# Kernel tuning notes

Hardware: AMD Instinct MI355X
Metric: run time of the kernel (lower is better)

Reference implementation:

```python
import jax, jax.numpy as jnp
import numpy as np

B, S, D, H, F, V, T, L = 64, 1024, 256, 256, 128, 50000, 64, 8
H2 = 2 * H
DIN = H2 + D + 3 * F  # 1152


def setup_inputs() -> dict:
    key = jax.random.key(0)
    ks = jax.random.split(key, 12)
    sd = 0.05
    return {
        "word_ids": jax.random.randint(ks[0], (B, S), 1, V, dtype=jnp.int32),
        "embed": jax.random.normal(ks[1], (V, D), jnp.float32) * sd,
        "encoder_outputs": jax.random.normal(ks[2], (B, S, H2), jnp.float32) * sd,
        "wconv1": jax.random.normal(ks[3], (F, 1, D), jnp.float32) * sd,
        "bconv1": jax.random.normal(ks[4], (F,), jnp.float32) * sd,
        "wconv2": jax.random.normal(ks[5], (F, 2, D), jnp.float32) * sd,
        "bconv2": jax.random.normal(ks[6], (F,), jnp.float32) * sd,
        "wconv3": jax.random.normal(ks[7], (F, 3, D), jnp.float32) * sd,
        "bconv3": jax.random.normal(ks[8], (F,), jnp.float32) * sd,
        "W_ih": jax.random.normal(ks[9], (4 * H2, DIN), jnp.float32) * sd,
        "W_hh": jax.random.normal(ks[10], (4 * H2, H2), jnp.float32) * sd,
        "W_fc": jax.random.normal(ks[11], (T, H2), jnp.float32) * sd,
        "seg_len": L,
    }


def reference(word_ids, embed, encoder_outputs, wconv1, bconv1, wconv2, bconv2,
              wconv3, bconv3, W_ih, W_hh, W_fc, seg_len):
    b, s = word_ids.shape
    d = embed.shape[1]
    h2 = encoder_outputs.shape[-1]
    h = h2 // 2
    nseg = s // seg_len

    # word features via embedding lookup (WordFeature with single 'word' feature)
    wf = embed[word_ids]                                  # [B, S, D]
    xs = wf.reshape(b, nseg, seg_len, d)                  # [B, nseg, L, D]
    c_w = xs.mean(axis=2)                                 # [B, nseg, D]
    es = encoder_outputs.reshape(b, nseg, seg_len, h2)
    c_h = es.mean(axis=2)                                 # [B, nseg, 2H]

    # char-CNN per segment: conv2d(1->F, (fs, D)) == 1D conv over time with D in-channels
    xc = xs.reshape(b * nseg, seg_len, d).transpose(0, 2, 1)  # [N, D, L]

    def conv_pool(w, bias):
        k = w.transpose(0, 2, 1)                          # [F, D, fs]
        y = jax.lax.conv_general_dilated(xc, k, window_strides=(1,),
                                         padding="VALID",
                                         dimension_numbers=("NCH", "OIH", "NCH"))
        y = jax.nn.relu(y + bias[None, :, None])
        return y.max(axis=2)                              # max-pool over time -> [N, F]

    c_x = jnp.concatenate([conv_pool(wconv1, bconv1),
                           conv_pool(wconv2, bconv2),
                           conv_pool(wconv3, bconv3)], axis=1)
    c_x = c_x.reshape(b, nseg, -1)                        # [B, nseg, 3F]

    dec_in = jnp.concatenate([c_w, c_h, c_x], axis=-1)    # [B, nseg, DIN]

    # decoder init: fwd-last / bwd-first encoder states
    h0 = jnp.concatenate([encoder_outputs[:, -1, :h], encoder_outputs[:, 0, h:]], axis=1)
    c0 = jnp.zeros_like(h0)

    def step(carry, x):
        hh, cc = carry
        gates = x @ W_ih.T + hh @ W_hh.T                  # [B, 4*2H]
        i, fg, g, o = jnp.split(gates, 4, axis=1)
        cc = jax.nn.sigmoid(fg) * cc + jax.nn.sigmoid(i) * jnp.tanh(g)
        hh = jax.nn.sigmoid(o) * jnp.tanh(cc)
        out = jax.nn.log_softmax(hh @ W_fc.T, axis=-1)
        return (hh, cc), out

    _, outs = jax.lax.scan(step, (h0, c0), dec_in.transpose(1, 0, 2))  # [nseg, B, T]
    return outs.transpose(1, 0, 2).reshape(b * nseg, -1)  # batch-major like the torch loop
```

## Files before the change

kernel.cpp:

```cpp
#include <hip/hip_runtime.h>
#include <math.h>

#define BB   64
#define SS   1024
#define DD   256
#define H2   512
#define FF   128
#define TT   64
#define NSEG 128
#define DIN  1152
#define G4   2048
#define MROWS 8192
#define MX   65536

typedef __attribute__((ext_vector_type(8))) short bf16x8;
typedef __attribute__((ext_vector_type(4))) float f32x4;

__device__ __forceinline__ unsigned short f2b(float f){
    union { float f; unsigned u; } v; v.f = f;
    unsigned r = v.u + 0x7fffu + ((v.u >> 16) & 1u);
    return (unsigned short)(r >> 16);
}
__device__ __forceinline__ float b2f(unsigned short h){
    union { unsigned u; float f; } v; v.u = ((unsigned)h) << 16;
    return v.f;
}
__device__ __forceinline__ float fsig(float x){
    return 1.f / (1.f + __expf(-x));
}
__device__ __forceinline__ float ftanh(float x){
    float e = __expf(-2.f * fabsf(x));
    float r = (1.f - e) / (1.f + e);
    return x < 0.f ? -r : r;
}


__global__ void k_cvt(const float* __restrict__ src, unsigned short* __restrict__ dst, int n){
    int i = blockIdx.x * 256 + threadIdx.x;
    if (i < n) dst[i] = f2b(src[i]);
}

__global__ void k_wf(const float* __restrict__ w1, const float* __restrict__ w2,
                     const float* __restrict__ w3, unsigned short* __restrict__ Wf){
    int i = blockIdx.x * 256 + threadIdx.x;
    int col = i >> 8, d = i & 255;
    float v;
    if (col < 128)      v = w1[col * 256 + d];
    else if (col < 384) { int f = (col - 128) & 127; int tap = (col - 128) >> 7; v = w2[f * 512 + tap * 256 + d]; }
    else                { int c = col - 384; int f = c & 127; int tap = c >> 7;  v = w3[f * 768 + tap * 256 + d]; }
    Wf[i] = f2b(v);
}

__global__ void k_tr_wfc(const float* __restrict__ src, float* __restrict__ dst){
    int i = blockIdx.x * 256 + threadIdx.x;
    int v = i >> 9, k = i & 511;
    dst[k * 64 + v] = src[i];
}

__global__ void k_gather(const int* __restrict__ wid, const float* __restrict__ embed,
                         unsigned short* __restrict__ X){
    int i = blockIdx.x * 256 + threadIdx.x;
    int row = i >> 6, d4 = i & 63;
    int w = wid[row];
    float4 v = *(const float4*)(embed + (size_t)w * DD + d4 * 4);
    ushort4 o; o.x = f2b(v.x); o.y = f2b(v.y); o.z = f2b(v.z); o.w = f2b(v.w);
    *(ushort4*)(X + (size_t)row * DD + d4 * 4) = o;
}

__global__ void k_cw(const unsigned short* __restrict__ X, unsigned short* __restrict__ dec){
    int i = blockIdx.x * 256 + threadIdx.x;
    int row = i >> 8, d = i & 255;
    const unsigned short* p = X + (size_t)row * 8 * DD + d;
    float s = 0.f;
#pragma unroll
    for (int t = 0; t < 8; t++) s += b2f(p[t * DD]);
    dec[(size_t)row * DIN + d] = f2b(s * 0.125f);
}

__global__ void k_ch(const float* __restrict__ enc, unsigned short* __restrict__ dec){
    int i = blockIdx.x * 256 + threadIdx.x;
    int row = i >> 9, c = i & 511;
    const float* p = enc + (size_t)row * 8 * H2 + c;
    float s = 0.f;
#pragma unroll
    for (int t = 0; t < 8; t++) s += p[t * H2];
    dec[(size_t)row * DIN + 256 + c] = f2b(s * 0.125f);
}

__global__ void k_h0(const float* __restrict__ enc, unsigned short* __restrict__ Hbuf){
    int i = blockIdx.x * 256 + threadIdx.x;
    int b = i >> 9, c = i & 511;
    float v = (c < 256) ? enc[(size_t)b * SS * H2 + (size_t)(SS - 1) * H2 + c]
                        : enc[(size_t)b * SS * H2 + c];
    v = fminf(fmaxf(v, -1.875f), 1.875f);
    Hbuf[(size_t)b * 512 + c] = f2b(v);
}

__global__ void k_fill(uint4* __restrict__ p){
    int i = blockIdx.x * 256 + threadIdx.x;
    uint4 v; v.x = v.y = v.z = v.w = 0x7FC07FC0u;
    p[i] = v;
}

__global__ __launch_bounds__(256) void gemm_conv_pool(
    const unsigned short* __restrict__ X, const unsigned short* __restrict__ Wf,
    const float* __restrict__ b1, const float* __restrict__ b2, const float* __restrict__ b3,
    unsigned short* __restrict__ dec)
{
    __shared__ unsigned short As[128][40];
    __shared__ unsigned short Bs[128][40];
    const int tid = threadIdx.x;
    const int m0 = blockIdx.x * 128;
    const int w = tid >> 6, lane = tid & 63;
    const int lm = lane & 15, quad = lane >> 4;
    const int wm = (w >> 1) * 64, wn = (w & 1) * 64;
    const int r0 = tid >> 2;
    const int kp = (tid & 3) * 8;

    const int woffs[3]  = {0, 128, 384};
    const int colofs[3] = {0, 128, 256};
    const float* biases[3] = {b1, b2, b3};

    for (int c = 0; c < 3; c++){
        const int taps = c + 1;
        const f32x4 z = {0.f, 0.f, 0.f, 0.f};
        f32x4 acc[4][4];
#pragma unroll
        for (int i = 0; i < 4; i++)
#pragma unroll
            for (int j = 0; j < 4; j++) acc[i][j] = z;

        for (int kc2 = 0; kc2 < taps * 256; kc2 += 32){
            int tap = kc2 >> 8, kc = kc2 & 255;
            int ra = m0 + r0 + tap;        if (ra > MX - 1) ra = MX - 1;
            int rb = m0 + 64 + r0 + tap;   if (rb > MX - 1) rb = MX - 1;
            int bw = woffs[c] + tap * 128;
            uint4 a0 = *(const uint4*)(X  + (size_t)ra * DD + kc + kp);
            uint4 a1 = *(const uint4*)(X  + (size_t)rb * DD + kc + kp);
            uint4 b0 = *(const uint4*)(Wf + (size_t)(bw + r0) * DD + kc + kp);
            uint4 b1v= *(const uint4*)(Wf + (size_t)(bw + 64 + r0) * DD + kc + kp);
            __syncthreads();
            *(uint4*)&As[r0][kp] = a0;
            *(uint4*)&As[64 + r0][kp] = a1;
            *(uint4*)&Bs[r0][kp] = b0;
            *(uint4*)&Bs[64 + r0][kp] = b1v;
            __syncthreads();
            bf16x8 af[4], bf[4];
#pragma unroll
            for (int mt = 0; mt < 4; mt++) af[mt] = *(const bf16x8*)&As[wm + mt * 16 + lm][quad * 8];
#pragma unroll
            for (int nt = 0; nt < 4; nt++) bf[nt] = *(const bf16x8*)&Bs[wn + nt * 16 + lm][quad * 8];
#pragma unroll
            for (int mt = 0; mt < 4; mt++)
#pragma unroll
                for (int nt = 0; nt < 4; nt++)
                    acc[mt][nt] = __builtin_amdgcn_mfma_f32_16x16x32_bf16(af[mt], bf[nt], acc[mt][nt], 0, 0, 0);
        }

        const int pmax = 8 - taps;
        const float* bias = biases[c];
#pragma unroll
        for (int nt = 0; nt < 4; nt++){
            int f = wn + nt * 16 + lm;
            float bv = bias[f];
#pragma unroll
            for (int mt = 0; mt < 4; mt++){
                float mx = -1e30f;
#pragma unroll
                for (int r = 0; r < 4; r++){
                    int p = (quad & 1) * 4 + r;
                    if (p <= pmax) mx = fmaxf(mx, acc[mt][nt][r]);
                }
                float po = __shfl_xor(mx, 16);
                mx = fmaxf(mx, po);
                if (!(quad & 1)){
                    int seg = (m0 >> 3) + (wm >> 3) + mt * 2 + (quad >> 1);
                    float o = fmaxf(mx + bv, 0.f);
                    dec[(size_t)seg * DIN + 768 + colofs[c] + f] = f2b(o);
                }
            }
        }
    }
}

__global__ __launch_bounds__(256) void gemm_bt_gates(
    const unsigned short* __restrict__ A, const unsigned short* __restrict__ Bm,
    unsigned short* __restrict__ C, int M, int N, int K)
{
    __shared__ unsigned short As[128][40];
    __shared__ unsigned short Bs[128][40];
    const int tid = threadIdx.x;
    const int m0 = blockIdx.y * 128, n0 = blockIdx.x * 128;
    const int w = tid >> 6, lane = tid & 63;
    const int lm = lane & 15, quad = lane >> 4;
    const int wm = (w >> 1) * 64, wn = (w & 1) * 64;

    const f32x4 z = {0.f, 0.f, 0.f, 0.f};
    f32x4 acc[4][4];
#pragma unroll
    for (int i = 0; i < 4; i++)
#pragma unroll
        for (int j = 0; j < 4; j++) acc[i][j] = z;

    const int r0 = tid >> 2;
    const int kp = (tid & 3) * 8;

    for (int kc = 0; kc < K; kc += 32){
        uint4 a0 = *(const uint4*)(A + (size_t)(m0 + r0) * K + kc + kp);
        uint4 a1 = *(const uint4*)(A + (size_t)(m0 + 64 + r0) * K + kc + kp);
        uint4 b0 = *(const uint4*)(Bm + (size_t)(n0 + r0) * K + kc + kp);
        uint4 b1 = *(const uint4*)(Bm + (size_t)(n0 + 64 + r0) * K + kc + kp);
        __syncthreads();
        *(uint4*)&As[r0][kp] = a0;
        *(uint4*)&As[64 + r0][kp] = a1;
        *(uint4*)&Bs[r0][kp] = b0;
        *(uint4*)&Bs[64 + r0][kp] = b1;
        __syncthreads();
        bf16x8 af[4], bf[4];
#pragma unroll
        for (int mt = 0; mt < 4; mt++) af[mt] = *(const bf16x8*)&As[wm + mt * 16 + lm][quad * 8];
#pragma unroll
        for (int nt = 0; nt < 4; nt++) bf[nt] = *(const bf16x8*)&Bs[wn + nt * 16 + lm][quad * 8];
#pragma unroll
        for (int mt = 0; mt < 4; mt++)
#pragma unroll
            for (int nt = 0; nt < 4; nt++)
                acc[mt][nt] = __builtin_amdgcn_mfma_f32_16x16x32_bf16(af[mt], bf[nt], acc[mt][nt], 0, 0, 0);
    }
#pragma unroll
    for (int mt = 0; mt < 4; mt++){
        int mrow = m0 + wm + mt * 16 + quad * 4;
#pragma unroll
        for (int nt = 0; nt < 4; nt++){
            int ncol = n0 + wn + nt * 16 + lm;
            int g = ncol >> 9, c = ncol & 511;
            int gb = c >> 5, hcl = c & 31;
            int n = hcl * 4 + g;
#pragma unroll
            for (int r = 0; r < 4; r++){
                int m = mrow + r;
                int b = m >> 7, t = m & 127;
                int grp = b >> 4, bl = b & 15;
                size_t dst = (((size_t)(grp * 16 + gb) * NSEG + t) * 128 + n) * 16 + bl;
                C[dst] = f2b(acc[mt][nt][r]);
            }
        }
    }
}

__global__ __attribute__((amdgpu_flat_work_group_size(512, 512), amdgpu_waves_per_eu(2, 2)))
void k_lstm(
    const unsigned short* __restrict__ gxt,
    const unsigned short* __restrict__ Whh,
    unsigned short* __restrict__ Hbuf)
{
    __shared__ unsigned short h_lds[2][16 * 512];

    const int tid = threadIdx.x;
    const int nb = blockIdx.x;
    const int grp = nb >> 4, gb = nb & 15;
    const int w = tid >> 6, lane = tid & 63, lm = lane & 15, quad = lane >> 4;
    const int g = lm & 3;

    bf16x8 wf[16];
    {
        int n = w * 16 + lm;
        const unsigned short* p = Whh + (size_t)((n & 3) * 512 + gb * 32 + (n >> 2)) * H2 + quad * 8;
#pragma unroll
        for (int ks = 0; ks < 16; ks++) wf[ks] = *(const bf16x8*)(p + ks * 32);
    }

    float cst[4] = {0.f, 0.f, 0.f, 0.f};

    union Chunk { unsigned long long q[2]; uint4 u4; };

    for (int t = 0; t < NSEG; t++){
#pragma unroll
        for (int ks = 0; ks < 16; ks++) asm volatile("" : "+v"(wf[ks]));

        const unsigned short* hsrc = Hbuf + (size_t)t * (BB * H2) + (size_t)grp * (16 * H2);
        Chunk ch[2];
#pragma unroll
        for (int j = 0; j < 2; j++){
            const unsigned long long* p = (const unsigned long long*)(hsrc + (size_t)(j * 512 + tid) * 8);
            ch[j].q[0] = __hip_atomic_load(p,     __ATOMIC_RELAXED, __HIP_MEMORY_SCOPE_AGENT);
            ch[j].q[1] = __hip_atomic_load(p + 1, __ATOMIC_RELAXED, __HIP_MEMORY_SCOPE_AGENT);
        }

        const unsigned short* gchunk = gxt + ((size_t)nb * NSEG + t) * 2048;
        ushort4 pr = *(const ushort4*)(gchunk + (w * 16 + lm) * 16 + quad * 4);

        unsigned pend = 0x3u;
        while (pend){
            unsigned np = 0;
#pragma unroll
            for (int j = 0; j < 2; j++){
                if (pend & (1u << j)){
                    if (((ch[j].q[0] | ch[j].q[1]) & 0x4000400040004000ULL) != 0ULL){
                        const unsigned long long* p = (const unsigned long long*)(hsrc + (size_t)(j * 512 + tid) * 8);
                        ch[j].q[0] = __hip_atomic_load(p,     __ATOMIC_RELAXED, __HIP_MEMORY_SCOPE_AGENT);
                        ch[j].q[1] = __hip_atomic_load(p + 1, __ATOMIC_RELAXED, __HIP_MEMORY_SCOPE_AGENT);
                        np |= 1u << j;
                    }
                }
            }
            pend = np;
            if (pend) __builtin_amdgcn_s_sleep(1);
        }

        char* hb = (char*)&h_lds[t & 1][0];
#pragma unroll
        for (int j = 0; j < 2; j++){
            unsigned addr = (unsigned)(j * 512 + tid) * 16u;
            addr ^= ((addr >> 10) & 7u) << 4;
            *(uint4*)(hb + addr) = ch[j].u4;
        }
        __syncthreads();

        const unsigned hrowb = (unsigned)lm << 10;
        const unsigned swz = (unsigned)(lm & 7) << 4;
        f32x4 acc0 = {0.f, 0.f, 0.f, 0.f}, acc1 = {0.f, 0.f, 0.f, 0.f};
#pragma unroll
        for (int ks = 0; ks < 16; ks += 2){
            unsigned colb0 = ((unsigned)ks << 6) + ((unsigned)quad << 4);
            unsigned colb1 = colb0 + 64u;
            bf16x8 av0 = *(const bf16x8*)(hb + ((hrowb + colb0) ^ swz));
            bf16x8 av1 = *(const bf16x8*)(hb + ((hrowb + colb1) ^ swz));
            acc0 = __builtin_amdgcn_mfma_f32_16x16x32_bf16(av0, wf[ks],     acc0, 0, 0, 0);
            acc1 = __builtin_amdgcn_mfma_f32_16x16x32_bf16(av1, wf[ks + 1], acc1, 0, 0, 0);
        }

        const unsigned short* prs = (const unsigned short*)&pr;
        unsigned short hv4[4];
#pragma unroll
        for (int r = 0; r < 4; r++){
            float a = acc0[r] + acc1[r] + b2f(prs[r]);
            float bsw = __shfl_xor(a, 1);
            float p  = (g & 1) ? bsw : a;
            float qq = (g & 1) ? a : bsw;
            float c2 = __shfl_xor(p, 2);
            float d2 = __shfl_xor(qq, 2);
            float iv = (g & 2) ? c2 : p;
            float gv = (g & 2) ? p  : c2;
            float fv = (g & 2) ? d2 : qq;
            float ov = (g & 2) ? qq : d2;
            float si = fsig(iv), sf = fsig(fv), so = fsig(ov);
            float cn = sf * cst[r] + si * ftanh(gv);
            cst[r] = cn;
            unsigned short hv = f2b(so * ftanh(cn));
            if (hv & 0x4000u) hv = 0;
            hv4[r] = hv;
        }

#pragma unroll
        for (int r = 0; r < 4; r++){
            unsigned v01 = (unsigned)hv4[r] | ((unsigned)(unsigned short)__shfl_xor((int)hv4[r], 4) << 16);
            unsigned v23 = (unsigned)__shfl_xor((int)v01, 8);
            unsigned long long outq = (unsigned long long)v01 | ((unsigned long long)v23 << 32);
            if (lm == 0){
                int bt = grp * 16 + quad * 4 + r;
                unsigned long long* dp = (unsigned long long*)
                    (Hbuf + (size_t)(t + 1) * (BB * H2) + (size_t)bt * H2 + gb * 32 + w * 4);
                __hip_atomic_store(dp, outq, __ATOMIC_RELAXED, __HIP_MEMORY_SCOPE_AGENT);
            }
        }
        asm volatile("" ::: "memory");
    }
}

__global__ __launch_bounds__(256) void k_out(
    const unsigned short* __restrict__ Hbuf, const float* __restrict__ Wt, float* __restrict__ out)
{
    __shared__ float hsh[4][H2];
    const int w = threadIdx.x >> 6, lane = threadIdx.x & 63;
    const int row = blockIdx.x * 4 + w;
    const int b = row >> 7, t = row & 127;
    const unsigned short* hp = Hbuf + (size_t)(t + 1) * (BB * H2) + (size_t)b * H2;
    uint4 hv = *(const uint4*)(hp + lane * 8);
    const unsigned short* hs = (const unsigned short*)&hv;
#pragma unroll
    for (int i = 0; i < 8; i++) hsh[w][lane * 8 + i] = b2f(hs[i]);
    __syncthreads();
    float acc = 0.f;
#pragma unroll 8
    for (int k = 0; k < H2; k++)
        acc = fmaf(hsh[w][k], Wt[k * 64 + lane], acc);
    float m = acc;
#pragma unroll
    for (int off = 32; off; off >>= 1) m = fmaxf(m, __shfl_xor(m, off));
    float e = expf(acc - m), s = e;
#pragma unroll
    for (int off = 32; off; off >>= 1) s += __shfl_xor(s, off);
    out[(size_t)row * TT + lane] = acc - m - logf(s);
}

extern "C" void kernel_launch(void* const* d_in, const int* in_sizes, int n_in,
                              void* d_out, int out_size, void* d_ws, size_t ws_size,
                              hipStream_t stream)
{
    const int*   wid = (const int*)d_in[0];
    const float* emb = (const float*)d_in[1];
    const float* enc = (const float*)d_in[2];
    const float* wc1 = (const float*)d_in[3];
    const float* bc1 = (const float*)d_in[4];
    const float* wc2 = (const float*)d_in[5];
    const float* bc2 = (const float*)d_in[6];
    const float* wc3 = (const float*)d_in[7];
    const float* bc3 = (const float*)d_in[8];
    const float* wih = (const float*)d_in[9];
    const float* whh = (const float*)d_in[10];
    const float* wfc = (const float*)d_in[11];

    char* ws = (char*)d_ws;
    size_t off = 0;
    auto alloc = [&](size_t bytes) -> void* {
        void* p = ws + off; off += (bytes + 255) & ~(size_t)255; return p;
    };
    unsigned short* X    = (unsigned short*)alloc((size_t)MX * DD * 2);
    unsigned short* dec  = (unsigned short*)alloc((size_t)MROWS * DIN * 2);
    unsigned short* Gb   = (unsigned short*)alloc((size_t)MX * 384 * 2);
    unsigned short* Wfb  = (unsigned short*)alloc((size_t)768 * 256 * 2);
    unsigned short* Wihb = (unsigned short*)alloc((size_t)G4 * DIN * 2);
    unsigned short* Whhb = (unsigned short*)alloc((size_t)G4 * H2 * 2);
    float*          Wfct = (float*)alloc((size_t)H2 * TT * 4);
    unsigned short* Hbuf  = X;
    unsigned short* gates = Gb;

    k_cvt<<<(G4 * DIN + 255) / 256, 256, 0, stream>>>(wih, Wihb, G4 * DIN);
    k_cvt<<<(G4 * H2 + 255) / 256, 256, 0, stream>>>(whh, Whhb, G4 * H2);
    k_wf<<<768, 256, 0, stream>>>(wc1, wc2, wc3, Wfb);
    k_tr_wfc<<<128, 256, 0, stream>>>(wfc, Wfct);
    k_gather<<<MX / 4, 256, 0, stream>>>(wid, emb, X);
    k_cw<<<MROWS, 256, 0, stream>>>(X, dec);
    k_ch<<<MROWS * 2, 256, 0, stream>>>(enc, dec);

    gemm_conv_pool<<<512, 256, 0, stream>>>(X, Wfb, bc1, bc2, bc3, dec);

    k_h0<<<BB * H2 / 256, 256, 0, stream>>>(enc, Hbuf);
    k_fill<<<2048, 256, 0, stream>>>((uint4*)(Hbuf + BB * H2));

    gemm_bt_gates<<<dim3(16, 64), 256, 0, stream>>>(dec, Wihb, gates, MROWS, G4, DIN);
    k_lstm<<<64, 512, 0, stream>>>(gates, Whhb, Hbuf);
    k_out<<<2048, 256, 0, stream>>>(Hbuf, Wfct, (float*)d_out);
}
```

Baseline: 1.060 ms.

## Fuse output projection and log-softmax into LSTM recurrence kernel

The separate output kernel and the W_fc transpose kernel are removed. Instead, wave 0 of each LSTM block computes the 64-way projection and log-softmax for the previous step's hidden row, read from LDS, and the loop runs one extra iteration to finish the last step. The gates GEMM now writes plain row-major output, and the LSTM gathers its per-step pre-activations with strided scalar loads instead of one contiguous vector load. This saves two launches and a re-read of Hbuf, but adds serial work inside the latency-bound recurrence and makes the gate loads less coalesced.

Measured after the change: 1.515 ms. 1.43x slower.

```diff
diff --git a/kernel.cpp b/kernel.cpp
--- a/kernel.cpp
+++ b/kernel.cpp
@@ -49,12 +49,6 @@
     else if (col < 384) { int f = (col - 128) & 127; int tap = (col - 128) >> 7; v = w2[f * 512 + tap * 256 + d]; }
     else                { int c = col - 384; int f = c & 127; int tap = c >> 7;  v = w3[f * 768 + tap * 256 + d]; }
     Wf[i] = f2b(v);
-}
-
-__global__ void k_tr_wfc(const float* __restrict__ src, float* __restrict__ dst){
-    int i = blockIdx.x * 256 + threadIdx.x;
-    int v = i >> 9, k = i & 511;
-    dst[k * 64 + v] = src[i];
 }
 
 __global__ void k_gather(const int* __restrict__ wid, const float* __restrict__ embed,
@@ -183,7 +177,7 @@
     }
 }
 
-__global__ __launch_bounds__(256) void gemm_bt_gates(
+__global__ __launch_bounds__(256) void gemm_bt(
     const unsigned short* __restrict__ A, const unsigned short* __restrict__ Bm,
     unsigned short* __restrict__ C, int M, int N, int K)
 {
@@ -233,17 +227,9 @@
 #pragma unroll
         for (int nt = 0; nt < 4; nt++){
             int ncol = n0 + wn + nt * 16 + lm;
-            int g = ncol >> 9, c = ncol & 511;
-            int gb = c >> 5, hcl = c & 31;
-            int n = hcl * 4 + g;
-#pragma unroll
-            for (int r = 0; r < 4; r++){
-                int m = mrow + r;
-                int b = m >> 7, t = m & 127;
-                int grp = b >> 4, bl = b & 15;
-                size_t dst = (((size_t)(grp * 16 + gb) * NSEG + t) * 128 + n) * 16 + bl;
-                C[dst] = f2b(acc[mt][nt][r]);
-            }
+#pragma unroll
+            for (int r = 0; r < 4; r++)
+                C[(size_t)(mrow + r) * N + ncol] = f2b(acc[mt][nt][r]);
         }
     }
 }
@@ -252,7 +238,9 @@
 void k_lstm(
     const unsigned short* __restrict__ gxt,
     const unsigned short* __restrict__ Whh,
-    unsigned short* __restrict__ Hbuf)
+    unsigned short* __restrict__ Hbuf,
+    const float* __restrict__ wfc,
+    float* __restrict__ out)
 {
     __shared__ unsigned short h_lds[2][16 * 512];
 
@@ -270,11 +258,13 @@
         for (int ks = 0; ks < 16; ks++) wf[ks] = *(const bf16x8*)(p + ks * 32);
     }
 
+    const int ncol_g = ((w * 16 + lm) & 3) * 512 + gb * 32 + ((w * 16 + lm) >> 2);
+
     float cst[4] = {0.f, 0.f, 0.f, 0.f};
 
     union Chunk { unsigned long long q[2]; uint4 u4; };
 
-    for (int t = 0; t < NSEG; t++){
+    for (int t = 0; t <= NSEG; t++){
 #pragma unroll
         for (int ks = 0; ks < 16; ks++) asm volatile("" : "+v"(wf[ks]));
 
@@ -287,8 +277,14 @@
             ch[j].q[1] = __hip_atomic_load(p + 1, __ATOMIC_RELAXED, __HIP_MEMORY_SCOPE_AGENT);
         }
 
-        const unsigned short* gchunk = gxt + ((size_t)nb * NSEG + t) * 2048;
-        ushort4 pr = *(const ushort4*)(gchunk + (w * 16 + lm) * 16 + quad * 4);
+        unsigned short prv[4];
+        if (t < NSEG){
+#pragma unroll
+            for (int r = 0; r < 4; r++){
+                int m = (grp * 16 + quad * 4 + r) * NSEG + t;
+                prv[r] = gxt[(size_t)m * G4 + ncol_g];
+            }
+        }
 
         unsigned pend = 0x3u;
         while (pend){
@@ -317,81 +313,87 @@
         }
         __syncthreads();
 
-        const unsigned hrowb = (unsigned)lm << 10;
-        const unsigned swz = (unsigned)(lm & 7) << 4;
-        f32x4 acc0 = {0.f, 0.f, 0.f, 0.f}, acc1 = {0.f, 0.f, 0.f, 0.f};
-#pragma unroll
-        for (int ks = 0; ks < 16; ks += 2){
-            unsigned colb0 = ((unsigned)ks << 6) + ((unsigned)quad << 4);
-            unsigned colb1 = colb0 + 64u;
-            bf16x8 av0 = *(const bf16x8*)(hb + ((hrowb + colb0) ^ swz));
-            bf16x8 av1 = *(const bf16x8*)(hb + ((hrowb + colb1) ^ swz));
-            acc0 = __builtin_amdgcn_mfma_f32_16x16x32_bf16(av0, wf[ks],     acc0, 0, 0, 0);
-            acc1 = __builtin_amdgcn_mfma_f32_16x16x32_bf16(av1, wf[ks + 1], acc1, 0, 0, 0);
-        }
-
-        const unsigned short* prs = (const unsigned short*)&pr;
-        unsigned short hv4[4];
-#pragma unroll
-        for (int r = 0; r < 4; r++){
-            float a = acc0[r] + acc1[r] + b2f(prs[r]);
-            float bsw = __shfl_xor(a, 1);
-            float p  = (g & 1) ? bsw : a;
-            float qq = (g & 1) ? a : bsw;
-            float c2 = __shfl_xor(p, 2);
-            float d2 = __shfl_xor(qq, 2);
-            float iv = (g & 2) ? c2 : p;
-            float gv = (g & 2) ? p  : c2;
-            float fv = (g & 2) ? d2 : qq;
-            float ov = (g & 2) ? qq : d2;
-            float si = fsig(iv), sf = fsig(fv), so = fsig(ov);
-            float cn = sf * cst[r] + si * ftanh(gv);
-            cst[r] = cn;
-            unsigned short hv = f2b(so * ftanh(cn));
-            if (hv & 0x4000u) hv = 0;
-            hv4[r] = hv;
-        }
-
-#pragma unroll
-        for (int r = 0; r < 4; r++){
-            unsigned v01 = (unsigned)hv4[r] | ((unsigned)(unsigned short)__shfl_xor((int)hv4[r], 4) << 16);
-            unsigned v23 = (unsigned)__shfl_xor((int)v01, 8);
-            unsigned long long outq = (unsigned long long)v01 | ((unsigned long long)v23 << 32);
-            if (lm == 0){
-                int bt = grp * 16 + quad * 4 + r;
-                unsigned long long* dp = (unsigned long long*)
-                    (Hbuf + (size_t)(t + 1) * (BB * H2) + (size_t)bt * H2 + gb * 32 + w * 4);
-                __hip_atomic_store(dp, outq, __ATOMIC_RELAXED, __HIP_MEMORY_SCOPE_AGENT);
-            }
+        if (t < NSEG){
+            const unsigned hrowb = (unsigned)lm << 10;
+            const unsigned swz = (unsigned)(lm & 7) << 4;
+            f32x4 acc0 = {0.f, 0.f, 0.f, 0.f}, acc1 = {0.f, 0.f, 0.f, 0.f};
+#pragma unroll
+            for (int ks = 0; ks < 16; ks += 2){
+                unsigned colb0 = ((unsigned)ks << 6) + ((unsigned)quad << 4);
+                unsigned colb1 = colb0 + 64u;
+                bf16x8 av0 = *(const bf16x8*)(hb + ((hrowb + colb0) ^ swz));
+                bf16x8 av1 = *(const bf16x8*)(hb + ((hrowb + colb1) ^ swz));
+                acc0 = __builtin_amdgcn_mfma_f32_16x16x32_bf16(av0, wf[ks],     acc0, 0, 0, 0);
+                acc1 = __builtin_amdgcn_mfma_f32_16x16x32_bf16(av1, wf[ks + 1], acc1, 0, 0, 0);
+            }
+
+            unsigned short hv4[4];
+#pragma unroll
+            for (int r = 0; r < 4; r++){
+                float a = acc0[r] + acc1[r] + b2f(prv[r]);
+                float bsw = __shfl_xor(a, 1);
+                float p  = (g & 1) ? bsw : a;
+                float qq = (g & 1) ? a : bsw;
+                float c2 = __shfl_xor(p, 2);
+                float d2 = __shfl_xor(qq, 2);
+                float iv = (g & 2) ? c2 : p;
+                float gv = (g & 2) ? p  : c2;
+                float fv = (g & 2) ? d2 : qq;
+                float ov = (g & 2) ? qq : d2;
+                float si = fsig(iv), sf = fsig(fv), so = fsig(ov);
+                float cn = sf * cst[r] + si * ftanh(gv);
+                cst[r] = cn;
+                unsigned short hv = f2b(so * ftanh(cn));
+                if (hv & 0x4000u) hv = 0;
+                hv4[r] = hv;
+            }
+
+#pragma unroll
+            for (int r = 0; r < 4; r++){
+                unsigned v01 = (unsigned)hv4[r] | ((unsigned)(unsigned short)__shfl_xor((int)hv4[r], 4) << 16);
+                unsigned v23 = (unsigned)__shfl_xor((int)v01, 8);
+                unsigned long long outq = (unsigned long long)v01 | ((unsigned long long)v23 << 32);
+                if (lm == 0){
+                    int bt = grp * 16 + quad * 4 + r;
+                    unsigned long long* dp = (unsigned long long*)
+                        (Hbuf + (size_t)(t + 1) * (BB * H2) + (size_t)bt * H2 + gb * 32 + w * 4);
+                    __hip_atomic_store(dp, outq, __ATOMIC_RELAXED, __HIP_MEMORY_SCOPE_AGENT);
+                }
+            }
+        }
+
+        if (w == 0 && t > 0){
+            const char* hbp = (const char*)&h_lds[t & 1][0];
+            const unsigned rowb = (unsigned)gb << 10;
+            const unsigned rx = (unsigned)(gb & 7) << 4;
+            const float* wrow = wfc + (size_t)lane * H2;
+            float accp = 0.f;
+#pragma unroll 8
+            for (int c16 = 0; c16 < 64; c16++){
+                bf16x8 hvv = *(const bf16x8*)(hbp + ((rowb + (unsigned)c16 * 16u) ^ rx));
+                float4 w0 = *(const float4*)(wrow + c16 * 8);
+                float4 w1 = *(const float4*)(wrow + c16 * 8 + 4);
+                const unsigned short* hs = (const unsigned short*)&hvv;
+                accp = fmaf(b2f(hs[0]), w0.x, accp);
+                accp = fmaf(b2f(hs[1]), w0.y, accp);
+                accp = fmaf(b2f(hs[2]), w0.z, accp);
+                accp = fmaf(b2f(hs[3]), w0.w, accp);
+                accp = fmaf(b2f(hs[4]), w1.x, accp);
+                accp = fmaf(b2f(hs[5]), w1.y, accp);
+                accp = fmaf(b2f(hs[6]), w1.z, accp);
+                accp = fmaf(b2f(hs[7]), w1.w, accp);
+            }
+            float mm = accp;
+#pragma unroll
+            for (int off = 32; off; off >>= 1) mm = fmaxf(mm, __shfl_xor(mm, off));
+            float e = expf(accp - mm), ss = e;
+#pragma unroll
+            for (int off = 32; off; off >>= 1) ss += __shfl_xor(ss, off);
+            int orow = (grp * 16 + gb) * NSEG + (t - 1);
+            out[(size_t)orow * TT + lane] = accp - mm - logf(ss);
         }
         asm volatile("" ::: "memory");
     }
-}
-
-__global__ __launch_bounds__(256) void k_out(
-    const unsigned short* __restrict__ Hbuf, const float* __restrict__ Wt, float* __restrict__ out)
-{
-    __shared__ float hsh[4][H2];
-    const int w = threadIdx.x >> 6, lane = threadIdx.x & 63;
-    const int row = blockIdx.x * 4 + w;
-    const int b = row >> 7, t = row & 127;
-    const unsigned short* hp = Hbuf + (size_t)(t + 1) * (BB * H2) + (size_t)b * H2;
-    uint4 hv = *(const uint4*)(hp + lane * 8);
-    const unsigned short* hs = (const unsigned short*)&hv;
-#pragma unroll
-    for (int i = 0; i < 8; i++) hsh[w][lane * 8 + i] = b2f(hs[i]);
-    __syncthreads();
-    float acc = 0.f;
-#pragma unroll 8
-    for (int k = 0; k < H2; k++)
-        acc = fmaf(hsh[w][k], Wt[k * 64 + lane], acc);
-    float m = acc;
-#pragma unroll
-    for (int off = 32; off; off >>= 1) m = fmaxf(m, __shfl_xor(m, off));
-    float e = expf(acc - m), s = e;
-#pragma unroll
-    for (int off = 32; off; off >>= 1) s += __shfl_xor(s, off);
-    out[(size_t)row * TT + lane] = acc - m - logf(s);
 }
 
 extern "C" void kernel_launch(void* const* d_in, const int* in_sizes, int n_in,
@@ -418,18 +420,16 @@
     };
     unsigned short* X    = (unsigned short*)alloc((size_t)MX * DD * 2);
     unsigned short* dec  = (unsigned short*)alloc((size_t)MROWS * DIN * 2);
-    unsigned short* Gb   = (unsigned short*)alloc((size_t)MX * 384 * 2);
+    unsigned short* Gb   = (unsigned short*)alloc((size_t)MROWS * G4 * 2);
     unsigned short* Wfb  = (unsigned short*)alloc((size_t)768 * 256 * 2);
     unsigned short* Wihb = (unsigned short*)alloc((size_t)G4 * DIN * 2);
     unsigned short* Whhb = (unsigned short*)alloc((size_t)G4 * H2 * 2);
-    float*          Wfct = (float*)alloc((size_t)H2 * TT * 4);
     unsigned short* Hbuf  = X;
     unsigned short* gates = Gb;
 
     k_cvt<<<(G4 * DIN + 255) / 256, 256, 0, stream>>>(wih, Wihb, G4 * DIN);
     k_cvt<<<(G4 * H2 + 255) / 256, 256, 0, stream>>>(whh, Whhb, G4 * H2);
     k_wf<<<768, 256, 0, stream>>>(wc1, wc2, wc3, Wfb);
-    k_tr_wfc<<<128, 256, 0, stream>>>(wfc, Wfct);
     k_gather<<<MX / 4, 256, 0, stream>>>(wid, emb, X);
     k_cw<<<MROWS, 256, 0, stream>>>(X, dec);
     k_ch<<<MROWS * 2, 256, 0, stream>>>(enc, dec);
@@ -439,7 +439,7 @@
     k_h0<<<BB * H2 / 256, 256, 0, stream>>>(enc, Hbuf);
     k_fill<<<2048, 256, 0, stream>>>((uint4*)(Hbuf + BB * H2));
 
-    gemm_bt_gates<<<dim3(16, 64), 256, 0, stream>>>(dec, Wihb, gates, MROWS, G4, DIN);
-    k_lstm<<<64, 512, 0, stream>>>(gates, Whhb, Hbuf);
-    k_out<<<2048, 256, 0, stream>>>(Hbuf, Wfct, (float*)d_out);
-}
+    gemm_bt<<<dim3(16, 64), 256, 0, stream>>>(dec, Wihb, gates, MROWS, G4, DIN);
+
+    k_lstm<<<64, 512, 0, stream>>>(gates, Whhb, Hbuf, wfc, (float*)d_out);
+}
```
